# Optimization experiments

Measured on AMD Instinct MI355X. Metric: run time of the kernel, lower is better.

Reference implementation:

```python
import jax, jax.numpy as jnp
import numpy as np


def _gather(feat, idx):
    # feat: [B, L, F], idx: [B, L, D] -> [B, L, D, F]  (per-molecule neighbor gather)
    return jax.vmap(lambda f, i: f[i])(feat, idx)


def setup_inputs() -> dict:
    key = jax.random.key(0)
    ks = jax.random.split(key, 16)
    B, L, D, F, FA, FB, R = 256, 128, 6, 200, 39, 10, 2
    s = 0.05
    return {
        "atom_list": jax.random.normal(ks[0], (B, L, FA), jnp.float32),
        "bond_list": jax.random.normal(ks[1], (B, L, FB), jnp.float32),
        "atom_degree": jax.random.randint(ks[2], (B, L, D), 0, L, jnp.int32),
        "bond_degree": jax.random.randint(ks[3], (B, L, D), 0, L, jnp.int32),
        "atom_W": jax.random.normal(ks[4], (F, FA), jnp.float32) * s,
        "atom_b": jax.random.normal(ks[5], (F,), jnp.float32) * s,
        "nbr_W": jax.random.normal(ks[6], (F, FA + FB), jnp.float32) * s,
        "nbr_b": jax.random.normal(ks[7], (F,), jnp.float32) * s,
        "align_W": jax.random.normal(ks[8], (R, 1, 2 * F), jnp.float32) * s,
        "align_b": jax.random.normal(ks[9], (R, 1), jnp.float32) * s,
        "attend_W": jax.random.normal(ks[10], (R, F, F), jnp.float32) * s,
        "attend_b": jax.random.normal(ks[11], (R, F), jnp.float32) * s,
        "gru_Wih": jax.random.normal(ks[12], (R, 3 * F, F), jnp.float32) * s,
        "gru_Whh": jax.random.normal(ks[13], (R, 3 * F, F), jnp.float32) * s,
        "gru_bih": jax.random.normal(ks[14], (R, 3 * F), jnp.float32) * s,
        "gru_bhh": jax.random.normal(ks[15], (R, 3 * F), jnp.float32) * s,
    }


def reference(atom_list, bond_list, atom_degree, bond_degree,
              atom_W, atom_b, nbr_W, nbr_b,
              align_W, align_b, attend_W, attend_b,
              gru_Wih, gru_Whh, gru_bih, gru_bhh):
    B, L, _ = atom_list.shape
    F = atom_W.shape[0]
    R = align_W.shape[0]
    pad = L - 1  # padding atom index convention from metaGAT

    # masks over padded neighbor slots: [B, L, D, 1]
    is_pad = (atom_degree == pad)[..., None]
    attend_mask = jnp.where(is_pad, 0.0, 1.0).astype(atom_list.dtype)
    softmax_mask = jnp.where(is_pad, -9e8, 0.0).astype(atom_list.dtype)

    # initial atom / neighbor embeddings
    atom_feat = jax.nn.leaky_relu(atom_list @ atom_W.T + atom_b)          # [B,L,F]
    atom_nbr = _gather(atom_list, atom_degree)                             # [B,L,D,FA]
    bond_nbr = _gather(bond_list, bond_degree)                             # [B,L,D,FB]
    nbr_feat = jax.nn.leaky_relu(
        jnp.concatenate([atom_nbr, bond_nbr], axis=-1) @ nbr_W.T + nbr_b)  # [B,L,D,F]

    cur = atom_feat  # GRU hidden / query features (activated after first step)
    for d in range(R):
        if d > 0:
            nbr_feat = _gather(cur, atom_degree)  # [B,L,D,F]
        cur_exp = jnp.broadcast_to(cur[:, :, None, :], nbr_feat.shape)
        feat_align = jnp.concatenate([cur_exp, nbr_feat], axis=-1)        # [B,L,D,2F]
        score = jax.nn.leaky_relu(feat_align @ align_W[d].T + align_b[d]) # [B,L,D,1]
        score = score + softmax_mask
        attn = jax.nn.softmax(score, axis=-2) * attend_mask               # [B,L,D,1]
        nbr_t = nbr_feat @ attend_W[d].T + attend_b[d]                    # [B,L,D,F]
        context = jax.nn.elu(jnp.sum(attn * nbr_t, axis=-2))              # [B,L,F]

        # GRUCell(input=context, hidden=cur)
        gi = context @ gru_Wih[d].T + gru_bih[d]                          # [B,L,3F]
        gh = cur @ gru_Whh[d].T + gru_bhh[d]                              # [B,L,3F]
        ir, iz, inn = jnp.split(gi, 3, axis=-1)
        hr, hz, hn = jnp.split(gh, 3, axis=-1)
        r = jax.nn.sigmoid(ir + hr)
        z = jax.nn.sigmoid(iz + hz)
        n = jnp.tanh(inn + r * hn)
        h = (1.0 - z) * n + z * cur
        cur = jax.nn.relu(h)  # activated_features for next step
    return cur
```

## Files before the change

### kernel.cpp

```cpp
#include <hip/hip_runtime.h>

#define B_     256
#define L_     128
#define D_     6
#define F_     200
#define FA_    39
#define FB_    10
#define PAD_   127
#define LMASK  127
#define NT     256
#define KC     (F_/4)
#define NTILE  16
#define NQ     (NTILE * D_)
#define NF     (B_ * L_ * F_)
#define MSZ    (F_ * F_)
#define NNODES (B_ * L_)
#define NPAIRS (NNODES * D_)
#define KP     224
#define KPP    232
#define KSTEPS 7
#define NTL    13
#define FRAG_TOTAL (14 * NTL * KSTEPS * 64)

typedef __attribute__((ext_vector_type(8))) short sh8;
typedef __attribute__((ext_vector_type(4))) float f32x4;

__device__ __forceinline__ float lrelu(float x) { return x >= 0.0f ? x : 0.01f * x; }
__device__ __forceinline__ float sigm(float x)  { return 1.0f / (1.0f + __expf(-x)); }
__device__ __forceinline__ unsigned short f2b(float x) {
    unsigned int u = __float_as_uint(x);
    unsigned int r = (u + 0x7FFFu + ((u >> 16) & 1u)) >> 16;
    return (unsigned short)r;
}
__device__ __forceinline__ uint2 pack4(float4 v) {
    uint2 p;
    p.x = (unsigned int)f2b(v.x) | ((unsigned int)f2b(v.y) << 16);
    p.y = (unsigned int)f2b(v.z) | ((unsigned int)f2b(v.w) << 16);
    return p;
}
#define AFRAG(arr, ks) (*(const sh8*)&arr[lane & 15][(ks) * 32 + ((lane >> 4) << 3)])
__device__ __forceinline__ sh8 bfrag(const unsigned short* __restrict__ WFr,
                                     int mat, int t, int ks, int lane) {
    return *(const sh8*)(WFr + ((((size_t)mat * NTL + t) * KSTEPS + ks) * 64 + lane) * 8);
}

#define PN2 64
__global__ __launch_bounds__(NT)
void prep_kernel(const float* __restrict__ atom_list, const float* __restrict__ bond_list,
                 const float* __restrict__ atom_W, const float* __restrict__ atom_b,
                 const float* __restrict__ nbr_W,
                 float* __restrict__ cur0, float* __restrict__ PA, float* __restrict__ PB)
{
    const int node0 = blockIdx.x * PN2;
    const int tid   = threadIdx.x;
    const int f     = tid;
    const bool valid = (f < F_);
    const int fc    = valid ? f : 0;

    __shared__ float wsh[F_ * (FA_ + FB_)];

    float wa[FA_];
    float wn[FA_ + FB_];

    for (int i = tid; i < F_ * FA_; i += NT) wsh[i] = atom_W[i];
    __syncthreads();
    #pragma unroll
    for (int k = 0; k < FA_; ++k) wa[k] = wsh[fc * FA_ + k];
    __syncthreads();
    for (int i = tid; i < F_ * (FA_ + FB_); i += NT) wsh[i] = nbr_W[i];
    __syncthreads();
    #pragma unroll
    for (int k = 0; k < FA_ + FB_; ++k) wn[k] = wsh[fc * (FA_ + FB_) + k];

    const float ab = atom_b[fc];

    for (int n = 0; n < PN2; ++n) {
        const float* __restrict__ ar = atom_list + (size_t)(node0 + n) * FA_;
        const float* __restrict__ br = bond_list + (size_t)(node0 + n) * FB_;
        float accA = ab, accPA = 0.0f, accPB = 0.0f;
        #pragma unroll
        for (int k = 0; k < FA_; ++k) {
            const float a = ar[k];
            accA  += a * wa[k];
            accPA += a * wn[k];
        }
        #pragma unroll
        for (int k = 0; k < FB_; ++k) accPB += br[k] * wn[FA_ + k];
        if (valid) {
            const size_t o = (size_t)(node0 + n) * F_ + f;
            cur0[o] = lrelu(accA);
            PA[o]   = accPA;
            PB[o]   = accPB;
        }
    }
}

__global__ void build_frags(const float* __restrict__ attend_W,
                            const float* __restrict__ gru_Wih,
                            const float* __restrict__ gru_Whh,
                            unsigned short* __restrict__ WF)
{
    const int i = blockIdx.x * blockDim.x + threadIdx.x;
    if (i >= FRAG_TOTAL) return;
    const int lane = i & 63;
    int rest = i >> 6;
    const int ks = rest % KSTEPS; rest /= KSTEPS;
    const int t  = rest % NTL;
    const int m  = rest / NTL;
    const int n  = t * 16 + (lane & 15);
    const int k0 = ks * 32 + ((lane >> 4) << 3);
    const int r = m / 7, tt = m - r * 7;
    const float* src;
    if (tt == 0)      src = attend_W + (size_t)r * MSZ;
    else if (tt <= 3) src = gru_Wih + ((size_t)r * 3 + (tt - 1)) * MSZ;
    else              src = gru_Whh + ((size_t)r * 3 + (tt - 4)) * MSZ;
    unsigned short o[8];
    #pragma unroll
    for (int j = 0; j < 8; ++j) {
        const int k = k0 + j;
        const float v = (n < F_ && k < F_) ? src[(size_t)n * F_ + k] : 0.0f;
        o[j] = f2b(v);
    }
    uint4 w;
    w.x = (unsigned int)o[0] | ((unsigned int)o[1] << 16);
    w.y = (unsigned int)o[2] | ((unsigned int)o[3] << 16);
    w.z = (unsigned int)o[4] | ((unsigned int)o[5] << 16);
    w.w = (unsigned int)o[6] | ((unsigned int)o[7] << 16);
    ((uint4*)WF)[i] = w;
}

#define SN 32
__global__ __launch_bounds__(NT)
void score2_kernel(const float* __restrict__ feat, const float* __restrict__ alW2,
                   float* __restrict__ s2)
{
    const int tid  = threadIdx.x;
    const int node = blockIdx.x * SN + (tid >> 3);
    const int sub  = tid & 7;
    const float* row = feat + (size_t)node * F_;
    float b = 0.0f;
    for (int k = sub; k < F_; k += 8) b += row[k] * alW2[k];
    b += __shfl_xor(b, 1, 8); b += __shfl_xor(b, 2, 8); b += __shfl_xor(b, 4, 8);
    if (sub == 0) s2[node] = b;
}

#define PPB 32
__global__ __launch_bounds__(NT)
void pair_score_kernel(const int* __restrict__ atom_degree,
                       const int* __restrict__ bond_degree,
                       const float* __restrict__ PA, const float* __restrict__ PB,
                       const float* __restrict__ alW2, const float* __restrict__ nbr_b,
                       float* __restrict__ s2p)
{
    __shared__ float w_s[F_], b_s[F_];
    const int tid = threadIdx.x;
    if (tid < F_) { w_s[tid] = alW2[tid]; b_s[tid] = nbr_b[tid]; }
    const int xcd = blockIdx.x & 7;
    const int j   = blockIdx.x >> 3;
    const int mol = (j / 24) * 8 + xcd;
    const int q0  = mol * (L_ * D_) + (j % 24) * PPB;
    const int q   = q0 + (tid >> 3);
    const int sub = tid & 7;
    const int nidx = atom_degree[q] & LMASK;
    const int bidx = bond_degree[q] & LMASK;
    const int bL   = mol * L_;
    const float4* pa4 = (const float4*)(PA + (size_t)(bL + nidx) * F_);
    const float4* pb4 = (const float4*)(PB + (size_t)(bL + bidx) * F_);
    __syncthreads();
    float s = 0.0f;
    for (int kk = sub; kk < KC; kk += 8) {
        const float4 pa = pa4[kk], pb = pb4[kk];
        const float4 w  = ((const float4*)w_s)[kk];
        const float4 bb = ((const float4*)b_s)[kk];
        s += lrelu(pa.x + pb.x + bb.x) * w.x + lrelu(pa.y + pb.y + bb.y) * w.y
           + lrelu(pa.z + pb.z + bb.z) * w.z + lrelu(pa.w + pb.w + bb.w) * w.w;
    }
    s += __shfl_xor(s, 1, 8); s += __shfl_xor(s, 2, 8); s += __shfl_xor(s, 4, 8);
    if (sub == 0) s2p[q] = s;
}

__global__ __launch_bounds__(NT, 4)
void round_kernel(
    const int*   __restrict__ atom_degree,
    const int*   __restrict__ bond_degree,
    const float* __restrict__ align_W,
    const float* __restrict__ align_b,
    const unsigned short* __restrict__ WF,
    const float* __restrict__ attend_b,
    const float* __restrict__ gru_bih,
    const float* __restrict__ gru_bhh,
    const float* __restrict__ nbr_b,
    const float* __restrict__ PA,
    const float* __restrict__ PB,
    const float* __restrict__ s2_tab,
    const float* __restrict__ cur_in,
    float*       __restrict__ dst,
    int mode)
{
    const int bid   = blockIdx.x;
    const int mol   = ((bid >> 6) << 3) | (bid & 7);
    const int tile  = (bid >> 3) & 7;
    const int node0 = mol * L_ + tile * NTILE;
    const int bL    = mol * L_;
    const int tid   = threadIdx.x;
    const int lane  = tid & 63;
    const int wave  = tid >> 6;

    __shared__ __align__(16) unsigned short curb  [NTILE][KPP];
    __shared__ __align__(16) unsigned short mixedb[NTILE][KPP];
    __shared__ __align__(16) unsigned short ctxb  [NTILE][KPP];
    __shared__ __align__(16) float nbrb_s[F_];
    __shared__ float sc_s [NQ];
    __shared__ float asum_s[NTILE];
    __shared__ float s1_s[NTILE];
    __shared__ int   nidx_s[NQ];
    __shared__ int   bidx_s[NQ];

    for (int idx = tid; idx < NTILE * (KP - F_); idx += NT) {
        const int n = idx / (KP - F_), k = F_ + idx % (KP - F_);
        curb[n][k] = 0; mixedb[n][k] = 0; ctxb[n][k] = 0;
    }

    if (tid < NQ) {
        const int n = tid / D_, j = tid - n * D_;
        nidx_s[tid] = atom_degree[(node0 + n) * D_ + j] & LMASK;
        bidx_s[tid] = (mode == 0) ? (bond_degree[(node0 + n) * D_ + j] & LMASK) : 0;
    }
    if (mode == 0 && tid < F_) nbrb_s[tid] = nbr_b[tid];

    for (int idx = tid; idx < NTILE * KC; idx += NT) {
        const int n = idx / KC, kk = idx - n * KC;
        const float4 v = ((const float4*)(cur_in + (size_t)(node0 + n) * F_))[kk];
        *(uint2*)&curb[n][kk * 4] = pack4(v);
    }

    {
        const int n = tid >> 4, sub = tid & 15;
        const float* crow = cur_in + (size_t)(node0 + n) * F_;
        float a = 0.0f;
        for (int f = sub; f < F_; f += 16) a += crow[f] * align_W[f];
        a += __shfl_xor(a, 1, 16); a += __shfl_xor(a, 2, 16);
        a += __shfl_xor(a, 4, 16); a += __shfl_xor(a, 8, 16);
        if (sub == 0) s1_s[n] = a;
    }
    __syncthreads();

    if (tid < NQ) {
        const int n = tid / D_;
        const float s2v = (mode == 0)
            ? s2_tab[(size_t)(node0 + n) * D_ + (tid - n * D_)]
            : s2_tab[bL + nidx_s[tid]];
        float sc = lrelu(s1_s[n] + s2v + align_b[0]);
        if (nidx_s[tid] == PAD_) sc += -9.0e8f;
        sc_s[tid] = sc;
    }
    __syncthreads();

    if (tid < NTILE) {
        float m = sc_s[tid * D_];
        #pragma unroll
        for (int j = 1; j < D_; ++j) m = fmaxf(m, sc_s[tid * D_ + j]);
        float ex[D_]; float ssum = 0.0f;
        #pragma unroll
        for (int j = 0; j < D_; ++j) { ex[j] = __expf(sc_s[tid * D_ + j] - m); ssum += ex[j]; }
        const float inv = 1.0f / ssum;
        float as = 0.0f;
        #pragma unroll
        for (int j = 0; j < D_; ++j) {
            const float a = (nidx_s[tid * D_ + j] == PAD_) ? 0.0f : ex[j] * inv;
            sc_s[tid * D_ + j] = a;
            as += a;
        }
        asum_s[tid] = as;
    }
    __syncthreads();

    for (int idx = tid; idx < NTILE * KC; idx += NT) {
        const int n = idx / KC, kk = idx - n * KC;
        float4 m4 = make_float4(0.f, 0.f, 0.f, 0.f);
        if (mode == 0) {
            const float4 bb4 = ((const float4*)nbrb_s)[kk];
            #pragma unroll
            for (int j = 0; j < D_; ++j) {
                const float a = sc_s[n * D_ + j];
                const float4 pa4 = ((const float4*)(PA + (size_t)(bL + nidx_s[n*D_+j]) * F_))[kk];
                const float4 pb4 = ((const float4*)(PB + (size_t)(bL + bidx_s[n*D_+j]) * F_))[kk];
                m4.x += a * lrelu(pa4.x + pb4.x + bb4.x);
                m4.y += a * lrelu(pa4.y + pb4.y + bb4.y);
                m4.z += a * lrelu(pa4.z + pb4.z + bb4.z);
                m4.w += a * lrelu(pa4.w + pb4.w + bb4.w);
            }
        } else {
            #pragma unroll
            for (int j = 0; j < D_; ++j) {
                const float a = sc_s[n * D_ + j];
                const float4 v = ((const float4*)(cur_in + (size_t)(bL + nidx_s[n*D_+j]) * F_))[kk];
                m4.x += a * v.x; m4.y += a * v.y; m4.z += a * v.z; m4.w += a * v.w;
            }
        }
        *(uint2*)&mixedb[n][kk * 4] = pack4(m4);
    }
    __syncthreads();

    for (int t = wave; t < NTL; t += 4) {
        f32x4 acc = {0.f, 0.f, 0.f, 0.f};
        #pragma unroll
        for (int ks = 0; ks < KSTEPS; ++ks)
            acc = __builtin_amdgcn_mfma_f32_16x16x32_bf16(
                AFRAG(mixedb, ks), bfrag(WF, 0, t, ks, lane), acc, 0, 0, 0);
        const int f = t * 16 + (lane & 15);
        if (f < F_) {
            const float bb = attend_b[f];
            #pragma unroll
            for (int rg = 0; rg < 4; ++rg) {
                const int node = ((lane >> 4) << 2) + rg;
                float c = acc[rg] + asum_s[node] * bb;
                c = (c > 0.0f) ? c : (__expf(c) - 1.0f);
                ctxb[node][f] = f2b(c);
            }
        }
    }
    __syncthreads();

    for (int t = wave; t < NTL; t += 4) {
        f32x4 ar = {0.f,0.f,0.f,0.f}, az = {0.f,0.f,0.f,0.f};
        f32x4 ani = {0.f,0.f,0.f,0.f}, anh = {0.f,0.f,0.f,0.f};
        #pragma unroll
        for (int ks = 0; ks < KSTEPS; ++ks) {
            const sh8 ac = AFRAG(ctxb, ks);
            const sh8 ah = AFRAG(curb, ks);
            ar  = __builtin_amdgcn_mfma_f32_16x16x32_bf16(ac, bfrag(WF,1,t,ks,lane), ar, 0,0,0);
            ar  = __builtin_amdgcn_mfma_f32_16x16x32_bf16(ah, bfrag(WF,4,t,ks,lane), ar, 0,0,0);
            az  = __builtin_amdgcn_mfma_f32_16x16x32_bf16(ac, bfrag(WF,2,t,ks,lane), az, 0,0,0);
            az  = __builtin_amdgcn_mfma_f32_16x16x32_bf16(ah, bfrag(WF,5,t,ks,lane), az, 0,0,0);
            ani = __builtin_amdgcn_mfma_f32_16x16x32_bf16(ac, bfrag(WF,3,t,ks,lane), ani, 0,0,0);
            anh = __builtin_amdgcn_mfma_f32_16x16x32_bf16(ah, bfrag(WF,6,t,ks,lane), anh, 0,0,0);
        }
        const int f = t * 16 + (lane & 15);
        if (f < F_) {
            const float bir = gru_bih[f],        bhr = gru_bhh[f];
            const float biz = gru_bih[F_ + f],   bhz = gru_bhh[F_ + f];
            const float bin = gru_bih[2*F_ + f], bhn = gru_bhh[2*F_ + f];
            #pragma unroll
            for (int rg = 0; rg < 4; ++rg) {
                const int node = ((lane >> 4) << 2) + rg;
                const float r  = sigm(ar[rg] + bir + bhr);
                const float z  = sigm(az[rg] + biz + bhz);
                const float nn = tanhf(ani[rg] + bin + r * (anh[rg] + bhn));
                const float cv = cur_in[(size_t)(node0 + node) * F_ + f];
                const float h  = (1.0f - z) * nn + z * cv;
                dst[(size_t)(node0 + node) * F_ + f] = fmaxf(h, 0.0f);
            }
        }
    }
}

extern "C" __attribute__((visibility("default")))
void kernel_launch(void* const* d_in, const int* in_sizes, int n_in,
                   void* d_out, int out_size, void* d_ws, size_t ws_size,
                   hipStream_t stream) {
    const float* atom_list = (const float*)d_in[0];
    const float* bond_list = (const float*)d_in[1];
    const int*   atom_deg  = (const int*)d_in[2];
    const int*   bond_deg  = (const int*)d_in[3];
    const float* atom_W    = (const float*)d_in[4];
    const float* atom_b    = (const float*)d_in[5];
    const float* nbr_W     = (const float*)d_in[6];
    const float* nbr_b     = (const float*)d_in[7];
    const float* align_W   = (const float*)d_in[8];
    const float* align_b   = (const float*)d_in[9];
    const float* attend_W  = (const float*)d_in[10];
    const float* attend_b  = (const float*)d_in[11];
    const float* gru_Wih   = (const float*)d_in[12];
    const float* gru_Whh   = (const float*)d_in[13];
    const float* gru_bih   = (const float*)d_in[14];
    const float* gru_bhh   = (const float*)d_in[15];

    float* ws   = (float*)d_ws;
    float* cur0 = ws;
    float* PA   = ws + (size_t)NF;
    float* PB   = ws + (size_t)2*NF;
    float* cur1 = ws + (size_t)3*NF;
    float* s2b  = ws + (size_t)4*NF;
    unsigned short* WF = (unsigned short*)(s2b + NNODES);
    float* s2p  = (float*)(WF + (size_t)FRAG_TOTAL * 8);
    float* out  = (float*)d_out;

    prep_kernel<<<dim3(NNODES / PN2), dim3(NT), 0, stream>>>(
        atom_list, bond_list, atom_W, atom_b, nbr_W, cur0, PA, PB);

    build_frags<<<dim3((FRAG_TOTAL + NT - 1) / NT), dim3(NT), 0, stream>>>(
        attend_W, gru_Wih, gru_Whh, WF);

    pair_score_kernel<<<dim3(NPAIRS / PPB), dim3(NT), 0, stream>>>(
        atom_deg, bond_deg, PA, PB, align_W + F_, nbr_b, s2p);

    const dim3 grid(NNODES / NTILE);
    const size_t rframe = (size_t)7 * NTL * KSTEPS * 64 * 8;

    round_kernel<<<grid, dim3(NT), 0, stream>>>(
        atom_deg, bond_deg, align_W, align_b,
        WF, attend_b, gru_bih, gru_bhh,
        nbr_b, PA, PB, s2p, cur0, cur1, 0);

    score2_kernel<<<dim3(NNODES / SN), dim3(NT), 0, stream>>>(
        cur1, align_W + 2 * F_ + F_, s2b);

    round_kernel<<<grid, dim3(NT), 0, stream>>>(
        atom_deg, bond_deg, align_W + 2 * F_, align_b + 1,
        WF + rframe, attend_b + F_, gru_bih + 3 * F_, gru_bhh + 3 * F_,
        nbr_b, PA, PB, s2b, cur1, out, 1);
}
```

Before: 383.6 us.

## Double round-kernel node tile to reuse weight fragments across two MFMA row groups

Raises the per-block node tile from 16 to 32 so each weight B-fragment loaded from global memory feeds two 16-row MFMA accumulations. This halves weight-fragment traffic per node in the attend and GRU GEMMs. B fragments are also software-prefetched one k-step ahead so load latency overlaps with the MFMAs. The block-to-molecule mapping, the align-score reduction width, the launch-bounds occupancy hint and the prep kernel's nodes per block are adjusted to match. The cost is more accumulator registers and fewer resident blocks per CU.

```diff
diff --git a/kernel.cpp b/kernel.cpp
--- a/kernel.cpp
+++ b/kernel.cpp
@@ -10,7 +10,7 @@
 #define LMASK  127
 #define NT     256
 #define KC     (F_/4)
-#define NTILE  16
+#define NTILE  32
 #define NQ     (NTILE * D_)
 #define NF     (B_ * L_ * F_)
 #define MSZ    (F_ * F_)
@@ -38,13 +38,14 @@
     p.y = (unsigned int)f2b(v.z) | ((unsigned int)f2b(v.w) << 16);
     return p;
 }
-#define AFRAG(arr, ks) (*(const sh8*)&arr[lane & 15][(ks) * 32 + ((lane >> 4) << 3)])
+#define AFRAG2(arr, ks, g) \
+    (*(const sh8*)&arr[(lane & 15) + ((g) << 4)][(ks) * 32 + ((lane >> 4) << 3)])
 __device__ __forceinline__ sh8 bfrag(const unsigned short* __restrict__ WFr,
                                      int mat, int t, int ks, int lane) {
     return *(const sh8*)(WFr + ((((size_t)mat * NTL + t) * KSTEPS + ks) * 64 + lane) * 8);
 }
 
-#define PN2 64
+#define PN2 32
 __global__ __launch_bounds__(NT)
 void prep_kernel(const float* __restrict__ atom_list, const float* __restrict__ bond_list,
                  const float* __restrict__ atom_W, const float* __restrict__ atom_b,
@@ -179,7 +180,7 @@
     if (sub == 0) s2p[q] = s;
 }
 
-__global__ __launch_bounds__(NT, 4)
+__global__ __launch_bounds__(NT, 3)
 void round_kernel(
     const int*   __restrict__ atom_degree,
     const int*   __restrict__ bond_degree,
@@ -198,8 +199,8 @@
     int mode)
 {
     const int bid   = blockIdx.x;
-    const int mol   = ((bid >> 6) << 3) | (bid & 7);
-    const int tile  = (bid >> 3) & 7;
+    const int mol   = ((bid >> 5) << 3) | (bid & 7);
+    const int tile  = (bid >> 3) & 3;
     const int node0 = mol * L_ + tile * NTILE;
     const int bL    = mol * L_;
     const int tid   = threadIdx.x;
@@ -235,12 +236,11 @@
     }
 
     {
-        const int n = tid >> 4, sub = tid & 15;
+        const int n = tid >> 3, sub = tid & 7;
         const float* crow = cur_in + (size_t)(node0 + n) * F_;
         float a = 0.0f;
-        for (int f = sub; f < F_; f += 16) a += crow[f] * align_W[f];
-        a += __shfl_xor(a, 1, 16); a += __shfl_xor(a, 2, 16);
-        a += __shfl_xor(a, 4, 16); a += __shfl_xor(a, 8, 16);
+        for (int f = sub; f < F_; f += 8) a += crow[f] * align_W[f];
+        a += __shfl_xor(a, 1, 8); a += __shfl_xor(a, 2, 8); a += __shfl_xor(a, 4, 8);
         if (sub == 0) s1_s[n] = a;
     }
     __syncthreads();
@@ -303,38 +303,63 @@
     __syncthreads();
 
     for (int t = wave; t < NTL; t += 4) {
-        f32x4 acc = {0.f, 0.f, 0.f, 0.f};
-        #pragma unroll
-        for (int ks = 0; ks < KSTEPS; ++ks)
-            acc = __builtin_amdgcn_mfma_f32_16x16x32_bf16(
-                AFRAG(mixedb, ks), bfrag(WF, 0, t, ks, lane), acc, 0, 0, 0);
+        f32x4 a0 = {0.f,0.f,0.f,0.f}, a1 = {0.f,0.f,0.f,0.f};
+        sh8 b0 = bfrag(WF, 0, t, 0, lane);
+        #pragma unroll
+        for (int ks = 0; ks < KSTEPS; ++ks) {
+            sh8 bn = b0;
+            if (ks + 1 < KSTEPS) bn = bfrag(WF, 0, t, ks + 1, lane);
+            a0 = __builtin_amdgcn_mfma_f32_16x16x32_bf16(AFRAG2(mixedb, ks, 0), b0, a0, 0,0,0);
+            a1 = __builtin_amdgcn_mfma_f32_16x16x32_bf16(AFRAG2(mixedb, ks, 1), b0, a1, 0,0,0);
+            b0 = bn;
+        }
         const int f = t * 16 + (lane & 15);
         if (f < F_) {
             const float bb = attend_b[f];
             #pragma unroll
             for (int rg = 0; rg < 4; ++rg) {
                 const int node = ((lane >> 4) << 2) + rg;
-                float c = acc[rg] + asum_s[node] * bb;
-                c = (c > 0.0f) ? c : (__expf(c) - 1.0f);
-                ctxb[node][f] = f2b(c);
+                float c0 = a0[rg] + asum_s[node] * bb;
+                c0 = (c0 > 0.0f) ? c0 : (__expf(c0) - 1.0f);
+                ctxb[node][f] = f2b(c0);
+                float c1 = a1[rg] + asum_s[node + 16] * bb;
+                c1 = (c1 > 0.0f) ? c1 : (__expf(c1) - 1.0f);
+                ctxb[node + 16][f] = f2b(c1);
             }
         }
     }
     __syncthreads();
 
     for (int t = wave; t < NTL; t += 4) {
-        f32x4 ar = {0.f,0.f,0.f,0.f}, az = {0.f,0.f,0.f,0.f};
-        f32x4 ani = {0.f,0.f,0.f,0.f}, anh = {0.f,0.f,0.f,0.f};
+        f32x4 ar0={0.f,0.f,0.f,0.f}, ar1={0.f,0.f,0.f,0.f};
+        f32x4 az0={0.f,0.f,0.f,0.f}, az1={0.f,0.f,0.f,0.f};
+        f32x4 ani0={0.f,0.f,0.f,0.f}, ani1={0.f,0.f,0.f,0.f};
+        f32x4 anh0={0.f,0.f,0.f,0.f}, anh1={0.f,0.f,0.f,0.f};
+        sh8 b1 = bfrag(WF,1,t,0,lane), b2 = bfrag(WF,2,t,0,lane), b3 = bfrag(WF,3,t,0,lane);
+        sh8 b4 = bfrag(WF,4,t,0,lane), b5 = bfrag(WF,5,t,0,lane), b6 = bfrag(WF,6,t,0,lane);
         #pragma unroll
         for (int ks = 0; ks < KSTEPS; ++ks) {
-            const sh8 ac = AFRAG(ctxb, ks);
-            const sh8 ah = AFRAG(curb, ks);
-            ar  = __builtin_amdgcn_mfma_f32_16x16x32_bf16(ac, bfrag(WF,1,t,ks,lane), ar, 0,0,0);
-            ar  = __builtin_amdgcn_mfma_f32_16x16x32_bf16(ah, bfrag(WF,4,t,ks,lane), ar, 0,0,0);
-            az  = __builtin_amdgcn_mfma_f32_16x16x32_bf16(ac, bfrag(WF,2,t,ks,lane), az, 0,0,0);
-            az  = __builtin_amdgcn_mfma_f32_16x16x32_bf16(ah, bfrag(WF,5,t,ks,lane), az, 0,0,0);
-            ani = __builtin_amdgcn_mfma_f32_16x16x32_bf16(ac, bfrag(WF,3,t,ks,lane), ani, 0,0,0);
-            anh = __builtin_amdgcn_mfma_f32_16x16x32_bf16(ah, bfrag(WF,6,t,ks,lane), anh, 0,0,0);
+            sh8 n1=b1, n2=b2, n3=b3, n4=b4, n5=b5, n6=b6;
+            if (ks + 1 < KSTEPS) {
+                n1 = bfrag(WF,1,t,ks+1,lane); n2 = bfrag(WF,2,t,ks+1,lane);
+                n3 = bfrag(WF,3,t,ks+1,lane); n4 = bfrag(WF,4,t,ks+1,lane);
+                n5 = bfrag(WF,5,t,ks+1,lane); n6 = bfrag(WF,6,t,ks+1,lane);
+            }
+            const sh8 ac0 = AFRAG2(ctxb, ks, 0), ac1 = AFRAG2(ctxb, ks, 1);
+            const sh8 ah0 = AFRAG2(curb, ks, 0), ah1 = AFRAG2(curb, ks, 1);
+            ar0  = __builtin_amdgcn_mfma_f32_16x16x32_bf16(ac0, b1, ar0, 0,0,0);
+            ar1  = __builtin_amdgcn_mfma_f32_16x16x32_bf16(ac1, b1, ar1, 0,0,0);
+            ar0  = __builtin_amdgcn_mfma_f32_16x16x32_bf16(ah0, b4, ar0, 0,0,0);
+            ar1  = __builtin_amdgcn_mfma_f32_16x16x32_bf16(ah1, b4, ar1, 0,0,0);
+            az0  = __builtin_amdgcn_mfma_f32_16x16x32_bf16(ac0, b2, az0, 0,0,0);
+            az1  = __builtin_amdgcn_mfma_f32_16x16x32_bf16(ac1, b2, az1, 0,0,0);
+            az0  = __builtin_amdgcn_mfma_f32_16x16x32_bf16(ah0, b5, az0, 0,0,0);
+            az1  = __builtin_amdgcn_mfma_f32_16x16x32_bf16(ah1, b5, az1, 0,0,0);
+            ani0 = __builtin_amdgcn_mfma_f32_16x16x32_bf16(ac0, b3, ani0, 0,0,0);
+            ani1 = __builtin_amdgcn_mfma_f32_16x16x32_bf16(ac1, b3, ani1, 0,0,0);
+            anh0 = __builtin_amdgcn_mfma_f32_16x16x32_bf16(ah0, b6, anh0, 0,0,0);
+            anh1 = __builtin_amdgcn_mfma_f32_16x16x32_bf16(ah1, b6, anh1, 0,0,0);
+            b1=n1; b2=n2; b3=n3; b4=n4; b5=n5; b6=n6;
         }
         const int f = t * 16 + (lane & 15);
         if (f < F_) {
@@ -344,12 +369,23 @@
             #pragma unroll
             for (int rg = 0; rg < 4; ++rg) {
                 const int node = ((lane >> 4) << 2) + rg;
-                const float r  = sigm(ar[rg] + bir + bhr);
-                const float z  = sigm(az[rg] + biz + bhz);
-                const float nn = tanhf(ani[rg] + bin + r * (anh[rg] + bhn));
-                const float cv = cur_in[(size_t)(node0 + node) * F_ + f];
-                const float h  = (1.0f - z) * nn + z * cv;
-                dst[(size_t)(node0 + node) * F_ + f] = fmaxf(h, 0.0f);
+                {
+                    const float r  = sigm(ar0[rg] + bir + bhr);
+                    const float z  = sigm(az0[rg] + biz + bhz);
+                    const float nn = tanhf(ani0[rg] + bin + r * (anh0[rg] + bhn));
+                    const float cv = cur_in[(size_t)(node0 + node) * F_ + f];
+                    const float h  = (1.0f - z) * nn + z * cv;
+                    dst[(size_t)(node0 + node) * F_ + f] = fmaxf(h, 0.0f);
+                }
+                {
+                    const int node2 = node + 16;
+                    const float r  = sigm(ar1[rg] + bir + bhr);
+                    const float z  = sigm(az1[rg] + biz + bhz);
+                    const float nn = tanhf(ani1[rg] + bin + r * (anh1[rg] + bhn));
+                    const float cv = cur_in[(size_t)(node0 + node2) * F_ + f];
+                    const float h  = (1.0f - z) * nn + z * cv;
+                    dst[(size_t)(node0 + node2) * F_ + f] = fmaxf(h, 0.0f);
+                }
             }
         }
     }
```

New measurement: 451.2 us. 17.6% more time.

## Store PA/PB and activations as bf16 to halve gather traffic

Applied to the files above, without the earlier changes.

The precomputed neighbor projections PA/PB and the per-round activations are now also written as bf16 copies. The pair-score and round kernels gather these bf16 rows with 16-byte loads, which halves the bytes moved by the random neighbor gathers, and the curb staging becomes a plain copy with no conversion. It also swaps tanhf for an exp-based tanh and halves the prep kernel's nodes per block. The cost is extra bf16 writes, a larger workspace layout and reduced precision in the attention and context path.

```diff
diff --git a/kernel.cpp b/kernel.cpp
--- a/kernel.cpp
+++ b/kernel.cpp
@@ -10,6 +10,7 @@
 #define LMASK  127
 #define NT     256
 #define KC     (F_/4)
+#define KC8    (F_/8)
 #define NTILE  16
 #define NQ     (NTILE * D_)
 #define NF     (B_ * L_ * F_)
@@ -27,16 +28,17 @@
 
 __device__ __forceinline__ float lrelu(float x) { return x >= 0.0f ? x : 0.01f * x; }
 __device__ __forceinline__ float sigm(float x)  { return 1.0f / (1.0f + __expf(-x)); }
+__device__ __forceinline__ float fast_tanh(float x) {
+    const float e = __expf(2.0f * x);
+    return 1.0f - 2.0f / (e + 1.0f);
+}
 __device__ __forceinline__ unsigned short f2b(float x) {
     unsigned int u = __float_as_uint(x);
     unsigned int r = (u + 0x7FFFu + ((u >> 16) & 1u)) >> 16;
     return (unsigned short)r;
 }
-__device__ __forceinline__ uint2 pack4(float4 v) {
-    uint2 p;
-    p.x = (unsigned int)f2b(v.x) | ((unsigned int)f2b(v.y) << 16);
-    p.y = (unsigned int)f2b(v.z) | ((unsigned int)f2b(v.w) << 16);
-    return p;
+__device__ __forceinline__ float b2f(unsigned short u) {
+    return __uint_as_float(((unsigned int)u) << 16);
 }
 #define AFRAG(arr, ks) (*(const sh8*)&arr[lane & 15][(ks) * 32 + ((lane >> 4) << 3)])
 __device__ __forceinline__ sh8 bfrag(const unsigned short* __restrict__ WFr,
@@ -44,12 +46,13 @@
     return *(const sh8*)(WFr + ((((size_t)mat * NTL + t) * KSTEPS + ks) * 64 + lane) * 8);
 }
 
-#define PN2 64
+#define PN2 32
 __global__ __launch_bounds__(NT)
 void prep_kernel(const float* __restrict__ atom_list, const float* __restrict__ bond_list,
                  const float* __restrict__ atom_W, const float* __restrict__ atom_b,
                  const float* __restrict__ nbr_W,
-                 float* __restrict__ cur0, float* __restrict__ PA, float* __restrict__ PB)
+                 float* __restrict__ cur0, unsigned short* __restrict__ cur0b,
+                 unsigned short* __restrict__ PA, unsigned short* __restrict__ PB)
 {
     const int node0 = blockIdx.x * PN2;
     const int tid   = threadIdx.x;
@@ -88,9 +91,11 @@
         for (int k = 0; k < FB_; ++k) accPB += br[k] * wn[FA_ + k];
         if (valid) {
             const size_t o = (size_t)(node0 + n) * F_ + f;
-            cur0[o] = lrelu(accA);
-            PA[o]   = accPA;
-            PB[o]   = accPB;
+            const float c = lrelu(accA);
+            cur0[o]  = c;
+            cur0b[o] = f2b(c);
+            PA[o]    = f2b(accPA);
+            PB[o]    = f2b(accPB);
         }
     }
 }
@@ -148,7 +153,8 @@
 __global__ __launch_bounds__(NT)
 void pair_score_kernel(const int* __restrict__ atom_degree,
                        const int* __restrict__ bond_degree,
-                       const float* __restrict__ PA, const float* __restrict__ PB,
+                       const unsigned short* __restrict__ PA,
+                       const unsigned short* __restrict__ PB,
                        const float* __restrict__ alW2, const float* __restrict__ nbr_b,
                        float* __restrict__ s2p)
 {
@@ -164,16 +170,17 @@
     const int nidx = atom_degree[q] & LMASK;
     const int bidx = bond_degree[q] & LMASK;
     const int bL   = mol * L_;
-    const float4* pa4 = (const float4*)(PA + (size_t)(bL + nidx) * F_);
-    const float4* pb4 = (const float4*)(PB + (size_t)(bL + bidx) * F_);
+    const unsigned short* pa = PA + (size_t)(bL + nidx) * F_;
+    const unsigned short* pb = PB + (size_t)(bL + bidx) * F_;
     __syncthreads();
     float s = 0.0f;
-    for (int kk = sub; kk < KC; kk += 8) {
-        const float4 pa = pa4[kk], pb = pb4[kk];
-        const float4 w  = ((const float4*)w_s)[kk];
-        const float4 bb = ((const float4*)b_s)[kk];
-        s += lrelu(pa.x + pb.x + bb.x) * w.x + lrelu(pa.y + pb.y + bb.y) * w.y
-           + lrelu(pa.z + pb.z + bb.z) * w.z + lrelu(pa.w + pb.w + bb.w) * w.w;
+    for (int kk = sub; kk < KC8; kk += 8) {
+        const sh8 pa8 = *(const sh8*)(pa + kk * 8);
+        const sh8 pb8 = *(const sh8*)(pb + kk * 8);
+        #pragma unroll
+        for (int e = 0; e < 8; ++e)
+            s += lrelu(b2f((unsigned short)pa8[e]) + b2f((unsigned short)pb8[e])
+                       + b_s[kk * 8 + e]) * w_s[kk * 8 + e];
     }
     s += __shfl_xor(s, 1, 8); s += __shfl_xor(s, 2, 8); s += __shfl_xor(s, 4, 8);
     if (sub == 0) s2p[q] = s;
@@ -190,11 +197,13 @@
     const float* __restrict__ gru_bih,
     const float* __restrict__ gru_bhh,
     const float* __restrict__ nbr_b,
-    const float* __restrict__ PA,
-    const float* __restrict__ PB,
+    const unsigned short* __restrict__ PAb,
+    const unsigned short* __restrict__ PBb,
     const float* __restrict__ s2_tab,
     const float* __restrict__ cur_in,
+    const unsigned short* __restrict__ cur_inb,
     float*       __restrict__ dst,
+    unsigned short* __restrict__ dstb,
     int mode)
 {
     const int bid   = blockIdx.x;
@@ -228,10 +237,10 @@
     }
     if (mode == 0 && tid < F_) nbrb_s[tid] = nbr_b[tid];
 
-    for (int idx = tid; idx < NTILE * KC; idx += NT) {
-        const int n = idx / KC, kk = idx - n * KC;
-        const float4 v = ((const float4*)(cur_in + (size_t)(node0 + n) * F_))[kk];
-        *(uint2*)&curb[n][kk * 4] = pack4(v);
+    for (int idx = tid; idx < NTILE * KC8; idx += NT) {
+        const int n = idx / KC8, kk = idx - n * KC8;
+        *(uint4*)&curb[n][kk * 8] =
+            *(const uint4*)(cur_inb + (size_t)(node0 + n) * F_ + kk * 8);
     }
 
     {
@@ -275,30 +284,39 @@
     }
     __syncthreads();
 
-    for (int idx = tid; idx < NTILE * KC; idx += NT) {
-        const int n = idx / KC, kk = idx - n * KC;
-        float4 m4 = make_float4(0.f, 0.f, 0.f, 0.f);
+    for (int idx = tid; idx < NTILE * KC8; idx += NT) {
+        const int n = idx / KC8, kk = idx - n * KC8;
+        const int c0 = kk * 8;
+        float m[8];
+        #pragma unroll
+        for (int e = 0; e < 8; ++e) m[e] = 0.0f;
         if (mode == 0) {
-            const float4 bb4 = ((const float4*)nbrb_s)[kk];
             #pragma unroll
             for (int j = 0; j < D_; ++j) {
                 const float a = sc_s[n * D_ + j];
-                const float4 pa4 = ((const float4*)(PA + (size_t)(bL + nidx_s[n*D_+j]) * F_))[kk];
-                const float4 pb4 = ((const float4*)(PB + (size_t)(bL + bidx_s[n*D_+j]) * F_))[kk];
-                m4.x += a * lrelu(pa4.x + pb4.x + bb4.x);
-                m4.y += a * lrelu(pa4.y + pb4.y + bb4.y);
-                m4.z += a * lrelu(pa4.z + pb4.z + bb4.z);
-                m4.w += a * lrelu(pa4.w + pb4.w + bb4.w);
+                const sh8 pa8 = *(const sh8*)(PAb + (size_t)(bL + nidx_s[n*D_+j]) * F_ + c0);
+                const sh8 pb8 = *(const sh8*)(PBb + (size_t)(bL + bidx_s[n*D_+j]) * F_ + c0);
+                #pragma unroll
+                for (int e = 0; e < 8; ++e)
+                    m[e] += a * lrelu(b2f((unsigned short)pa8[e])
+                                    + b2f((unsigned short)pb8[e]) + nbrb_s[c0 + e]);
             }
         } else {
             #pragma unroll
             for (int j = 0; j < D_; ++j) {
                 const float a = sc_s[n * D_ + j];
-                const float4 v = ((const float4*)(cur_in + (size_t)(bL + nidx_s[n*D_+j]) * F_))[kk];
-                m4.x += a * v.x; m4.y += a * v.y; m4.z += a * v.z; m4.w += a * v.w;
+                const sh8 v8 = *(const sh8*)(cur_inb + (size_t)(bL + nidx_s[n*D_+j]) * F_ + c0);
+                #pragma unroll
+                for (int e = 0; e < 8; ++e)
+                    m[e] += a * b2f((unsigned short)v8[e]);
             }
         }
-        *(uint2*)&mixedb[n][kk * 4] = pack4(m4);
+        uint4 w;
+        w.x = (unsigned int)f2b(m[0]) | ((unsigned int)f2b(m[1]) << 16);
+        w.y = (unsigned int)f2b(m[2]) | ((unsigned int)f2b(m[3]) << 16);
+        w.z = (unsigned int)f2b(m[4]) | ((unsigned int)f2b(m[5]) << 16);
+        w.w = (unsigned int)f2b(m[6]) | ((unsigned int)f2b(m[7]) << 16);
+        *(uint4*)&mixedb[n][c0] = w;
     }
     __syncthreads();
 
@@ -346,10 +364,12 @@
                 const int node = ((lane >> 4) << 2) + rg;
                 const float r  = sigm(ar[rg] + bir + bhr);
                 const float z  = sigm(az[rg] + biz + bhz);
-                const float nn = tanhf(ani[rg] + bin + r * (anh[rg] + bhn));
-                const float cv = cur_in[(size_t)(node0 + node) * F_ + f];
-                const float h  = (1.0f - z) * nn + z * cv;
-                dst[(size_t)(node0 + node) * F_ + f] = fmaxf(h, 0.0f);
+                const float nn = fast_tanh(ani[rg] + bin + r * (anh[rg] + bhn));
+                const size_t o = (size_t)(node0 + node) * F_ + f;
+                const float cv = cur_in[o];
+                const float h  = fmaxf((1.0f - z) * nn + z * cv, 0.0f);
+                dst[o] = h;
+                if (mode == 0) dstb[o] = f2b(h);
             }
         }
     }
@@ -378,22 +398,24 @@
 
     float* ws   = (float*)d_ws;
     float* cur0 = ws;
-    float* PA   = ws + (size_t)NF;
-    float* PB   = ws + (size_t)2*NF;
-    float* cur1 = ws + (size_t)3*NF;
-    float* s2b  = ws + (size_t)4*NF;
-    unsigned short* WF = (unsigned short*)(s2b + NNODES);
-    float* s2p  = (float*)(WF + (size_t)FRAG_TOTAL * 8);
+    float* cur1 = ws + (size_t)NF;
+    float* s2b  = ws + (size_t)2*NF;
+    float* s2p  = s2b + NNODES;
+    unsigned short* cur0b = (unsigned short*)(s2p + NPAIRS);
+    unsigned short* cur1b = cur0b + (size_t)NF;
+    unsigned short* PAb   = cur1b + (size_t)NF;
+    unsigned short* PBb   = PAb   + (size_t)NF;
+    unsigned short* WF    = PBb   + (size_t)NF;
     float* out  = (float*)d_out;
 
     prep_kernel<<<dim3(NNODES / PN2), dim3(NT), 0, stream>>>(
-        atom_list, bond_list, atom_W, atom_b, nbr_W, cur0, PA, PB);
+        atom_list, bond_list, atom_W, atom_b, nbr_W, cur0, cur0b, PAb, PBb);
 
     build_frags<<<dim3((FRAG_TOTAL + NT - 1) / NT), dim3(NT), 0, stream>>>(
         attend_W, gru_Wih, gru_Whh, WF);
 
     pair_score_kernel<<<dim3(NPAIRS / PPB), dim3(NT), 0, stream>>>(
-        atom_deg, bond_deg, PA, PB, align_W + F_, nbr_b, s2p);
+        atom_deg, bond_deg, PAb, PBb, align_W + F_, nbr_b, s2p);
 
     const dim3 grid(NNODES / NTILE);
     const size_t rframe = (size_t)7 * NTL * KSTEPS * 64 * 8;
@@ -401,7 +423,7 @@
     round_kernel<<<grid, dim3(NT), 0, stream>>>(
         atom_deg, bond_deg, align_W, align_b,
         WF, attend_b, gru_bih, gru_bhh,
-        nbr_b, PA, PB, s2p, cur0, cur1, 0);
+        nbr_b, PAb, PBb, s2p, cur0, cur0b, cur1, cur1b, 0);
 
     score2_kernel<<<dim3(NNODES / SN), dim3(NT), 0, stream>>>(
         cur1, align_W + 2 * F_ + F_, s2b);
@@ -409,5 +431,5 @@
     round_kernel<<<grid, dim3(NT), 0, stream>>>(
         atom_deg, bond_deg, align_W + 2 * F_, align_b + 1,
         WF + rframe, attend_b + F_, gru_bih + 3 * F_, gru_bhh + 3 * F_,
-        nbr_b, PA, PB, s2b, cur1, out, 1);
-}
+        nbr_b, PAb, PBb, s2b, cur1, cur1b, out, nullptr, 1);
+}
```

New measurement: 356.3 us. -7.1%, faster.
